# Kernel tuning notes

Measured on AMD Instinct MI355X. Metric: run time of the kernel, lower is better.

## Reference

```python
import jax, jax.numpy as jnp
import numpy as np

N_NODES = 100000
N_EDGES = 600000
DIM = 128
NUM_CLASSES = 10
NUM_GRAPHS = 512
NUM_LAYERS = 4
BN_EPS = 1e-5


def _bn(h, g, b):
    # BatchNorm1d, training-mode statistics (biased variance), affine
    m = h.mean(axis=0)
    v = jnp.var(h, axis=0)
    return (h - m) * jax.lax.rsqrt(v + BN_EPS) * g + b


def setup_inputs() -> dict:
    key = jax.random.key(0)
    ks = jax.random.split(key, 8)
    s_in = 1.0 / np.sqrt(DIM)
    x = jax.random.normal(ks[0], (N_NODES, DIM), dtype=jnp.float32)
    edge_index = jax.random.randint(ks[1], (2, N_EDGES), 0, N_NODES, dtype=jnp.int32)
    batch = jnp.sort(jax.random.randint(ks[2], (N_NODES,), 0, NUM_GRAPHS, dtype=jnp.int32))
    return {
        "x": x,
        "edge_index": edge_index,
        "batch": batch,
        "mlp_w1": jax.random.normal(ks[3], (NUM_LAYERS, DIM, DIM), dtype=jnp.float32) * s_in,
        "mlp_b1": jnp.zeros((NUM_LAYERS, DIM), dtype=jnp.float32),
        "mlp_bn_g": jnp.ones((NUM_LAYERS, DIM), dtype=jnp.float32),
        "mlp_bn_b": jnp.zeros((NUM_LAYERS, DIM), dtype=jnp.float32),
        "mlp_w2": jax.random.normal(ks[4], (NUM_LAYERS, DIM, DIM), dtype=jnp.float32) * s_in,
        "mlp_b2": jnp.zeros((NUM_LAYERS, DIM), dtype=jnp.float32),
        "bn_g": jnp.ones((NUM_LAYERS, DIM), dtype=jnp.float32),
        "bn_b": jnp.zeros((NUM_LAYERS, DIM), dtype=jnp.float32),
        "fc_w": jax.random.normal(ks[5], (NUM_LAYERS + 1, DIM, NUM_CLASSES), dtype=jnp.float32) * s_in,
        "fc_b": jnp.zeros((NUM_LAYERS + 1, NUM_CLASSES), dtype=jnp.float32),
    }


def reference(x, edge_index, batch, mlp_w1, mlp_b1, mlp_bn_g, mlp_bn_b,
              mlp_w2, mlp_b2, bn_g, bn_b, fc_w, fc_b):
    src, dst = edge_index[0], edge_index[1]
    outs = [x]
    h = x
    for i in range(NUM_LAYERS):
        # GINConv: (1+eps)*x + sum_{j in N(i)} x_j  with eps=0 (default)
        agg = jax.ops.segment_sum(h[src], dst, num_segments=N_NODES)
        z = h + agg
        # nn.Sequential(Linear, BatchNorm1d, ReLU, Linear)
        z = jax.nn.relu(_bn(z @ mlp_w1[i] + mlp_b1[i], mlp_bn_g[i], mlp_bn_b[i]))
        z = z @ mlp_w2[i] + mlp_b2[i]
        # outer BN + ReLU
        h = jax.nn.relu(_bn(z, bn_g[i], bn_b[i]))
        outs.append(h)
    out = None
    for i, o in enumerate(outs):
        pooled = jax.ops.segment_sum(o, batch, num_segments=NUM_GRAPHS)
        y = pooled @ fc_w[i] + fc_b[i]  # dropout is identity in eval mode
        out = y if out is None else out + y
    return jax.nn.log_softmax(out, axis=-1)
```

## Files before the change

kernel.cpp:

```cpp
#include <hip/hip_runtime.h>

#define NN 100000
#define NE 600000
#define DD 128
#define NG 512
#define NC 10
#define NL 4

typedef __attribute__((ext_vector_type(8))) short short8;
typedef __attribute__((ext_vector_type(4))) float f32x4;

__device__ __forceinline__ float b2f(unsigned int u) { return __uint_as_float(u << 16); }
__device__ __forceinline__ unsigned int f2b(float f) {
    unsigned int u = __float_as_uint(f);
    return (u + 0x7fffu + ((u >> 16) & 1u)) >> 16;
}
__device__ __forceinline__ void unpack8(uint4 v, float* f) {
    f[0] = b2f(v.x & 0xffffu); f[1] = b2f(v.x >> 16);
    f[2] = b2f(v.y & 0xffffu); f[3] = b2f(v.y >> 16);
    f[4] = b2f(v.z & 0xffffu); f[5] = b2f(v.z >> 16);
    f[6] = b2f(v.w & 0xffffu); f[7] = b2f(v.w >> 16);
}
__device__ __forceinline__ uint4 pack8(const float* f) {
    uint4 v;
    v.x = f2b(f[0]) | (f2b(f[1]) << 16);
    v.y = f2b(f[2]) | (f2b(f[3]) << 16);
    v.z = f2b(f[4]) | (f2b(f[5]) << 16);
    v.w = f2b(f[6]) | (f2b(f[7]) << 16);
    return v;
}


__global__ __launch_bounds__(256) void k_zero(float* __restrict__ p, int n) {
    int i = blockIdx.x * 256 + threadIdx.x;
    if (i < n) p[i] = 0.f;
}
__global__ __launch_bounds__(256) void k_zeroint(int* __restrict__ p, int n) {
    int i = blockIdx.x * 256 + threadIdx.x;
    if (i < n) p[i] = 0;
}
__global__ __launch_bounds__(256) void k_copyint(const int* __restrict__ s, int* __restrict__ d, int n) {
    int i = blockIdx.x * 256 + threadIdx.x;
    if (i < n) d[i] = s[i];
}

__global__ __launch_bounds__(256) void k_cvtH(const float* __restrict__ x, ushort* __restrict__ h) {
    int i = blockIdx.x * 256 + threadIdx.x;
    if (i >= NN * DD / 8) return;
    float4 a = ((const float4*)x)[2 * i], b = ((const float4*)x)[2 * i + 1];
    float f[8] = {a.x, a.y, a.z, a.w, b.x, b.y, b.z, b.w};
    ((uint4*)h)[i] = pack8(f);
}

__global__ __launch_bounds__(256) void k_wpack(const float* __restrict__ w1, const float* __restrict__ w2,
                                               ushort* __restrict__ wp) {
    int id = blockIdx.x * 256 + threadIdx.x;
    int v = id & 63;
    int kc = (id >> 6) & 3;
    int ct = (id >> 8) & 7;
    int m = id >> 11;
    const float* W = (m < 4) ? (w1 + (size_t)m * DD * DD) : (w2 + (size_t)(m - 4) * DD * DD);
    int c = ct * 16 + (v & 15);
    int kbase = kc * 32 + ((v >> 4) << 3);
    ushort* dst = wp + ((size_t)id << 3);
    #pragma unroll
    for (int j = 0; j < 8; ++j) dst[j] = (ushort)f2b(W[(size_t)(kbase + j) * DD + c]);
}


__global__ __launch_bounds__(256) void k_hist(const int* __restrict__ dst, int* __restrict__ deg) {
    int e = blockIdx.x * 256 + threadIdx.x;
    if (e < NE) atomicAdd(&deg[dst[e]], 1);
}
__global__ __launch_bounds__(256) void k_partial(const int* __restrict__ deg, int* __restrict__ part) {
    __shared__ int s[256];
    int t = threadIdx.x;
    int i = blockIdx.x * 256 + t;
    s[t] = (i < NN) ? deg[i] : 0;
    __syncthreads();
    #pragma unroll
    for (int off = 128; off >= 1; off >>= 1) {
        if (t < off) s[t] += s[t + off];
        __syncthreads();
    }
    if (t == 0) part[blockIdx.x] = s[0];
}
__global__ __launch_bounds__(512) void k_scanpart(int* __restrict__ part, int nb) {
    __shared__ int s[512];
    int t = threadIdx.x;
    int v = (t < nb) ? part[t] : 0;
    s[t] = v;
    __syncthreads();
    #pragma unroll
    for (int off = 1; off < 512; off <<= 1) {
        int add = (t >= off) ? s[t - off] : 0;
        __syncthreads();
        s[t] += add;
        __syncthreads();
    }
    if (t < nb) part[t] = s[t] - v;
}
__global__ __launch_bounds__(256) void k_exscan(const int* __restrict__ deg, const int* __restrict__ part,
                                                int* __restrict__ rowofs) {
    __shared__ int s[256];
    int b = blockIdx.x, t = threadIdx.x;
    int i = b * 256 + t;
    int v = (i < NN) ? deg[i] : 0;
    s[t] = v;
    __syncthreads();
    #pragma unroll
    for (int off = 1; off < 256; off <<= 1) {
        int add = (t >= off) ? s[t - off] : 0;
        __syncthreads();
        s[t] += add;
        __syncthreads();
    }
    if (i < NN) rowofs[i] = part[b] + s[t] - v;
    if (i == NN - 1) rowofs[NN] = part[b] + s[t];
}
__global__ __launch_bounds__(256) void k_fill(const int* __restrict__ src, const int* __restrict__ dst,
                                              int* __restrict__ cursor, int* __restrict__ csr) {
    int e = blockIdx.x * 256 + threadIdx.x;
    if (e >= NE) return;
    int d = dst[e];
    int pos = atomicAdd(&cursor[d], 1);
    csr[pos] = src[e];
}

template<bool BN>
__global__ __launch_bounds__(256) void k_gather(const int* __restrict__ rowofs, const int* __restrict__ csr,
                                                const ushort* __restrict__ h, ushort* __restrict__ z,
                                                const float* __restrict__ scsh) {
    int t = threadIdx.x;
    int n = blockIdx.x * 16 + (t >> 4);
    int cl = t & 15;
    int cb = cl * 8;
    float sc[8], sh[8];
    if (BN) {
        #pragma unroll
        for (int j = 0; j < 8; ++j) { sc[j] = scsh[cb + j]; sh[j] = scsh[DD + cb + j]; }
    }
    float acc[8], f[8];
    uint4 v = ((const uint4*)h)[(size_t)n * 16 + cl];
    unpack8(v, f);
    #pragma unroll
    for (int j = 0; j < 8; ++j)
        acc[j] = BN ? fmaxf(fmaf(f[j], sc[j], sh[j]), 0.f) : f[j];
    int start = rowofs[n], end = rowofs[n + 1];
    for (int e = start; e < end; ++e) {
        int s = csr[e];
        v = ((const uint4*)h)[(size_t)s * 16 + cl];
        unpack8(v, f);
        #pragma unroll
        for (int j = 0; j < 8; ++j)
            acc[j] += BN ? fmaxf(fmaf(f[j], sc[j], sh[j]), 0.f) : f[j];
    }
    ((uint4*)z)[(size_t)n * 16 + cl] = pack8(acc);
}

template<bool TRANS>
__global__ __launch_bounds__(256, 4) void k_mm(const ushort* __restrict__ in, const ushort* __restrict__ wp,
                                               const float* __restrict__ bias, const float* __restrict__ scsh,
                                               ushort* __restrict__ outp,
                                               float* __restrict__ ssum, float* __restrict__ ssq) {
    __shared__ __align__(16) char lds[16384];
    const int t = threadIdx.x;
    const int lane = t & 63;
    const int wid = t >> 6;
    const int wr = wid >> 1, wc = wid & 1;
    const int rb = blockIdx.x * 64;
    const int rep = blockIdx.x & 7;

    float scv[8], shv[8];
    if (TRANS) {
        int cb = (t & 15) * 8;
        #pragma unroll
        for (int j = 0; j < 8; ++j) { scv[j] = scsh[cb + j]; shv[j] = scsh[DD + cb + j]; }
    }
    #pragma unroll
    for (int i = 0; i < 4; ++i) {
        int c = i * 256 + t;
        int row = c >> 4;
        int g = rb + row;
        uint4 v = make_uint4(0, 0, 0, 0);
        if (g < NN) {
            v = *((const uint4*)in + (size_t)g * 16 + (c & 15));
            if (TRANS) {
                float f[8];
                unpack8(v, f);
                #pragma unroll
                for (int j = 0; j < 8; ++j) f[j] = fmaxf(fmaf(f[j], scv[j], shv[j]), 0.f);
                v = pack8(f);
            }
        }
        *(uint4*)(lds + ((c * 16) ^ ((row & 7) << 4))) = v;
    }
    __syncthreads();

    f32x4 acc[2][4];
    #pragma unroll
    for (int rt = 0; rt < 2; ++rt)
        #pragma unroll
        for (int ct = 0; ct < 4; ++ct) acc[rt][ct] = (f32x4){0.f, 0.f, 0.f, 0.f};

    #pragma unroll
    for (int kc = 0; kc < 4; ++kc) {
        short8 wf[4];
        #pragma unroll
        for (int ct = 0; ct < 4; ++ct)
            wf[ct] = *(const short8*)(wp + (size_t)((((wc * 4 + ct) * 4 + kc) * 64 + lane) << 3));
        #pragma unroll
        for (int rt = 0; rt < 2; ++rt) {
            int row = wr * 32 + rt * 16 + (lane & 15);
            int off = (row * 256 + ((kc * 32 + ((lane >> 4) << 3)) << 1)) ^ ((row & 7) << 4);
            short8 zf = *(const short8*)(lds + off);
            #pragma unroll
            for (int ct = 0; ct < 4; ++ct)
                acc[rt][ct] = __builtin_amdgcn_mfma_f32_16x16x32_bf16(wf[ct], zf, acc[rt][ct], 0, 0, 0);
        }
    }
    __syncthreads();

    const int zr = lane & 15, cq = lane >> 4;
    #pragma unroll
    for (int rt = 0; rt < 2; ++rt) {
        int row = wr * 32 + rt * 16 + zr;
        #pragma unroll
        for (int ct = 0; ct < 4; ++ct) {
            int c0 = wc * 64 + ct * 16 + cq * 4;
            float4 bi = *(const float4*)(bias + c0);
            f32x4 a = acc[rt][ct];
            float v0 = a[0] + bi.x, v1 = a[1] + bi.y, v2 = a[2] + bi.z, v3 = a[3] + bi.w;
            uint2 pk;
            pk.x = f2b(v0) | (f2b(v1) << 16);
            pk.y = f2b(v2) | (f2b(v3) << 16);
            *(uint2*)(lds + ((row * 256 + c0 * 2) ^ ((row & 7) << 4))) = pk;
        }
    }
    __syncthreads();

    float s8[8], q8[8];
    #pragma unroll
    for (int j = 0; j < 8; ++j) { s8[j] = 0.f; q8[j] = 0.f; }
    #pragma unroll
    for (int i = 0; i < 4; ++i) {
        int c = i * 256 + t;
        int row = c >> 4;
        int g = rb + row;
        if (g < NN) {
            uint4 v = *(const uint4*)(lds + ((c * 16) ^ ((row & 7) << 4)));
            ((uint4*)outp)[(size_t)g * 16 + (c & 15)] = v;
            float f[8];
            unpack8(v, f);
            #pragma unroll
            for (int j = 0; j < 8; ++j) { s8[j] += f[j]; q8[j] += f[j] * f[j]; }
        }
    }
    __syncthreads();
    float* rs = (float*)lds;
    float* rq = rs + 16 * DD;
    const int slot = t >> 4, cb2 = (t & 15) * 8;
    #pragma unroll
    for (int j = 0; j < 8; j += 4) {
        *(float4*)(rs + slot * DD + cb2 + j) = make_float4(s8[j], s8[j + 1], s8[j + 2], s8[j + 3]);
        *(float4*)(rq + slot * DD + cb2 + j) = make_float4(q8[j], q8[j + 1], q8[j + 2], q8[j + 3]);
    }
    __syncthreads();
    #pragma unroll
    for (int off = 8; off >= 1; off >>= 1) {
        if (slot < off) {
            #pragma unroll
            for (int j = 0; j < 8; j += 4) {
                float4 a = *(float4*)(rs + slot * DD + cb2 + j);
                float4 b = *(float4*)(rs + (slot + off) * DD + cb2 + j);
                a.x += b.x; a.y += b.y; a.z += b.z; a.w += b.w;
                *(float4*)(rs + slot * DD + cb2 + j) = a;
                float4 c2 = *(float4*)(rq + slot * DD + cb2 + j);
                float4 d  = *(float4*)(rq + (slot + off) * DD + cb2 + j);
                c2.x += d.x; c2.y += d.y; c2.z += d.z; c2.w += d.w;
                *(float4*)(rq + slot * DD + cb2 + j) = c2;
            }
        }
        __syncthreads();
    }
    if (t < DD) {
        atomicAdd(ssum + rep * DD + t, rs[t]);
        atomicAdd(ssq + rep * DD + t, rq[t]);
    }
}

__global__ __launch_bounds__(DD) void k_finstats(float* __restrict__ ssum, float* __restrict__ ssq,
                                                 float* __restrict__ dst,
                                                 const float* __restrict__ g, const float* __restrict__ b) {
    int t = threadIdx.x;
    float s = 0.f, q = 0.f;
    #pragma unroll
    for (int r = 0; r < 8; ++r) {
        s += ssum[r * DD + t]; q += ssq[r * DD + t];
        ssum[r * DD + t] = 0.f; ssq[r * DD + t] = 0.f;
    }
    const float invn = 1.0f / NN;
    float m = s * invn;
    float var = q * invn - m * m;
    float sc = g[t] * rsqrtf(var + 1e-5f);
    dst[t] = sc;
    dst[DD + t] = b[t] - m * sc;
}

__device__ __forceinline__ int lowerb(const int* __restrict__ a, int n, int key) {
    int lo = 0, hi = n;
    while (lo < hi) {
        int mid = (lo + hi) >> 1;
        if (a[mid] < key) lo = mid + 1; else hi = mid;
    }
    return lo;
}

template<bool BN>
__global__ __launch_bounds__(256) void k_pool(const int* __restrict__ batch, const ushort* __restrict__ h,
                                              float* __restrict__ pooled, const float* __restrict__ scsh) {
    int g = blockIdx.x;
    int t = threadIdx.x;
    int cl = t & 15;
    int rs = t >> 4;
    int cb = cl * 8;
    float sc[8], sh[8];
    if (BN) {
        #pragma unroll
        for (int j = 0; j < 8; ++j) { sc[j] = scsh[cb + j]; sh[j] = scsh[DD + cb + j]; }
    }
    int start = lowerb(batch, NN, g);
    int end = lowerb(batch, NN, g + 1);
    float acc[8];
    #pragma unroll
    for (int j = 0; j < 8; ++j) acc[j] = 0.f;
    for (int n = start + rs; n < end; n += 16) {
        uint4 v = ((const uint4*)h)[(size_t)n * 16 + cl];
        float f[8];
        unpack8(v, f);
        #pragma unroll
        for (int j = 0; j < 8; ++j)
            acc[j] += BN ? fmaxf(fmaf(f[j], sc[j], sh[j]), 0.f) : f[j];
    }
    __shared__ float red[16 * DD];
    #pragma unroll
    for (int j = 0; j < 8; j += 4)
        *(float4*)(red + rs * DD + cb + j) = make_float4(acc[j], acc[j + 1], acc[j + 2], acc[j + 3]);
    __syncthreads();
    #pragma unroll
    for (int off = 8; off >= 1; off >>= 1) {
        if (rs < off) {
            #pragma unroll
            for (int j = 0; j < 8; j += 4) {
                float4 a = *(float4*)(red + rs * DD + cb + j);
                float4 b = *(float4*)(red + (rs + off) * DD + cb + j);
                a.x += b.x; a.y += b.y; a.z += b.z; a.w += b.w;
                *(float4*)(red + rs * DD + cb + j) = a;
            }
        }
        __syncthreads();
    }
    if (rs == 0) {
        #pragma unroll
        for (int j = 0; j < 8; j += 4)
            *(float4*)(pooled + (size_t)g * DD + cb + j) = *(float4*)(red + cb + j);
    }
}

__global__ __launch_bounds__(64) void k_readout(const float* __restrict__ pooled, const float* __restrict__ fcw,
                                                const float* __restrict__ fcb, float* __restrict__ out) {
    int g = blockIdx.x, t = threadIdx.x;
    float part[NC];
    #pragma unroll
    for (int c = 0; c < NC; ++c) part[c] = 0.f;
    for (int i = 0; i < NL + 1; ++i) {
        #pragma unroll
        for (int hh = 0; hh < 2; ++hh) {
            int d = t + (hh << 6);
            float v = pooled[((size_t)i * NG + g) * DD + d];
            const float* wr = fcw + ((size_t)i * DD + d) * NC;
            #pragma unroll
            for (int c = 0; c < NC; ++c) part[c] = fmaf(v, wr[c], part[c]);
        }
    }
    #pragma unroll
    for (int off = 32; off >= 1; off >>= 1) {
        #pragma unroll
        for (int c = 0; c < NC; ++c) part[c] += __shfl_down(part[c], off);
    }
    if (t == 0) {
        float y[NC];
        #pragma unroll
        for (int c = 0; c < NC; ++c) {
            float bs = 0.f;
            for (int i = 0; i < NL + 1; ++i) bs += fcb[i * NC + c];
            y[c] = part[c] + bs;
        }
        float m = y[0];
        #pragma unroll
        for (int c = 1; c < NC; ++c) m = fmaxf(m, y[c]);
        float sum = 0.f;
        #pragma unroll
        for (int c = 0; c < NC; ++c) sum += expf(y[c] - m);
        float ls = logf(sum);
        #pragma unroll
        for (int c = 0; c < NC; ++c) out[(size_t)g * NC + c] = y[c] - m - ls;
    }
}


extern "C" void kernel_launch(void* const* d_in, const int* in_sizes, int n_in,
                              void* d_out, int out_size, void* d_ws, size_t ws_size,
                              hipStream_t stream) {
    const float* x   = (const float*)d_in[0];
    const int*   ei  = (const int*)d_in[1];
    const int*   bat = (const int*)d_in[2];
    const float* w1  = (const float*)d_in[3];
    const float* b1  = (const float*)d_in[4];
    const float* mbg = (const float*)d_in[5];
    const float* mbb = (const float*)d_in[6];
    const float* w2  = (const float*)d_in[7];
    const float* b2  = (const float*)d_in[8];
    const float* bng = (const float*)d_in[9];
    const float* bnb = (const float*)d_in[10];
    const float* fcw = (const float*)d_in[11];
    const float* fcb = (const float*)d_in[12];
    float* out = (float*)d_out;

    ushort* H  = (ushort*)d_ws;
    ushort* Z  = H + (size_t)NN * DD;
    ushort* Y1 = Z + (size_t)NN * DD;
    ushort* WP = Y1 + (size_t)NN * DD;
    float* pooled = (float*)(WP + 8 * 16384);
    float* scsh   = pooled + (size_t)(NL + 1) * NG * DD;
    float* ssum   = scsh + NL * 2 * 2 * DD;
    float* ssq    = ssum + 8 * DD;
    int* deg    = (int*)(ssq + 8 * DD);
    int* rowofs = deg + NN;
    int* part   = rowofs + NN + 1;
    int* cursor = part + 512;
    int* csr    = cursor + NN;

    const int* src = ei;
    const int* dst = ei + NE;
    const int nbN = (NN + 255) / 256;
    const int nbE = (NE + 255) / 256;

    hipLaunchKernelGGL(k_cvtH, dim3(NN * DD / 8 / 256 + 1), dim3(256), 0, stream, x, H);
    hipLaunchKernelGGL(k_zero, dim3(8), dim3(256), 0, stream, ssum, 16 * DD);
    hipLaunchKernelGGL(k_zeroint, dim3(nbN), dim3(256), 0, stream, deg, NN);
    hipLaunchKernelGGL(k_hist, dim3(nbE), dim3(256), 0, stream, dst, deg);
    hipLaunchKernelGGL(k_partial, dim3(nbN), dim3(256), 0, stream, deg, part);
    hipLaunchKernelGGL(k_scanpart, dim3(1), dim3(512), 0, stream, part, nbN);
    hipLaunchKernelGGL(k_exscan, dim3(nbN), dim3(256), 0, stream, deg, part, rowofs);
    hipLaunchKernelGGL(k_copyint, dim3(nbN), dim3(256), 0, stream, rowofs, cursor, NN);
    hipLaunchKernelGGL(k_fill, dim3(nbE), dim3(256), 0, stream, src, dst, cursor, csr);
    hipLaunchKernelGGL(k_wpack, dim3(64), dim3(256), 0, stream, w1, w2, WP);

    const int gmm = (NN + 63) / 64;
    for (int i = 0; i < NL; ++i) {
        float* slot_mlp = scsh + (size_t)(i * 2 + 0) * 2 * DD;
        float* slot_out = scsh + (size_t)(i * 2 + 1) * 2 * DD;
        if (i == 0) {
            hipLaunchKernelGGL((k_pool<false>), dim3(NG), dim3(256), 0, stream, bat, H, pooled, (const float*)nullptr);
            hipLaunchKernelGGL((k_gather<false>), dim3(NN / 16), dim3(256), 0, stream, rowofs, csr, H, Z, (const float*)nullptr);
        } else {
            const float* bnp = scsh + (size_t)((i - 1) * 2 + 1) * 2 * DD;
            hipLaunchKernelGGL((k_pool<true>), dim3(NG), dim3(256), 0, stream, bat, H, pooled + (size_t)i * NG * DD, bnp);
            hipLaunchKernelGGL((k_gather<true>), dim3(NN / 16), dim3(256), 0, stream, rowofs, csr, H, Z, bnp);
        }
        hipLaunchKernelGGL((k_mm<false>), dim3(gmm), dim3(256), 0, stream,
                           Z, WP + (size_t)i * 16384, b1 + (size_t)i * DD, (const float*)nullptr, Y1, ssum, ssq);
        hipLaunchKernelGGL(k_finstats, dim3(1), dim3(DD), 0, stream, ssum, ssq, slot_mlp, mbg + (size_t)i * DD, mbb + (size_t)i * DD);
        hipLaunchKernelGGL((k_mm<true>), dim3(gmm), dim3(256), 0, stream,
                           Y1, WP + (size_t)(4 + i) * 16384, b2 + (size_t)i * DD, slot_mlp, H, ssum, ssq);
        hipLaunchKernelGGL(k_finstats, dim3(1), dim3(DD), 0, stream, ssum, ssq, slot_out, bng + (size_t)i * DD, bnb + (size_t)i * DD);
    }
    hipLaunchKernelGGL((k_pool<true>), dim3(NG), dim3(256), 0, stream, bat, H,
                       pooled + (size_t)NL * NG * DD, scsh + (size_t)(3 * 2 + 1) * 2 * DD);
    hipLaunchKernelGGL(k_readout, dim3(NG), dim3(64), 0, stream, pooled, fcw, fcb, out);
}
```

Baseline: 453.5 us.

## Fuse neighbor gather, graph pooling and first MLP matmul into one kernel

```diff
diff --git a/kernel.cpp b/kernel.cpp
--- a/kernel.cpp
+++ b/kernel.cpp
@@ -128,34 +128,171 @@
 }
 
 template<bool BN>
-__global__ __launch_bounds__(256) void k_gather(const int* __restrict__ rowofs, const int* __restrict__ csr,
-                                                const ushort* __restrict__ h, ushort* __restrict__ z,
-                                                const float* __restrict__ scsh) {
-    int t = threadIdx.x;
-    int n = blockIdx.x * 16 + (t >> 4);
-    int cl = t & 15;
-    int cb = cl * 8;
-    float sc[8], sh[8];
+__global__ __launch_bounds__(256, 4) void k_gmm(const ushort* __restrict__ h,
+                                                const int* __restrict__ rowofs, const int* __restrict__ csr,
+                                                const int* __restrict__ batch,
+                                                const ushort* __restrict__ wp, const float* __restrict__ bias,
+                                                const float* __restrict__ scsh,
+                                                ushort* __restrict__ outp,
+                                                float* __restrict__ ssum, float* __restrict__ ssq,
+                                                float* __restrict__ poolslot) {
+    __shared__ __align__(16) char lds[16384];
+    __shared__ float plds[8][DD];
+    const int t = threadIdx.x;
+    const int lane = t & 63;
+    const int wid = t >> 6;
+    const int wr = wid >> 1, wc = wid & 1;
+    const int rb = blockIdx.x * 64;
+    const int rep = blockIdx.x & 7;
+    const int cl = t & 15, cb = cl * 8;
+
+    const int g0 = batch[rb];
+    const int gr = batch[min(rb + 63, NN - 1)] - g0;
+    const bool direct = (gr >= 8);
+    if (!direct) {
+        for (int i = t; i < 8 * DD; i += 256) ((float*)plds)[i] = 0.f;
+    }
+    float scv[8], shv[8];
     if (BN) {
         #pragma unroll
-        for (int j = 0; j < 8; ++j) { sc[j] = scsh[cb + j]; sh[j] = scsh[DD + cb + j]; }
-    }
-    float acc[8], f[8];
-    uint4 v = ((const uint4*)h)[(size_t)n * 16 + cl];
-    unpack8(v, f);
-    #pragma unroll
-    for (int j = 0; j < 8; ++j)
-        acc[j] = BN ? fmaxf(fmaf(f[j], sc[j], sh[j]), 0.f) : f[j];
-    int start = rowofs[n], end = rowofs[n + 1];
-    for (int e = start; e < end; ++e) {
-        int s = csr[e];
-        v = ((const uint4*)h)[(size_t)s * 16 + cl];
-        unpack8(v, f);
-        #pragma unroll
-        for (int j = 0; j < 8; ++j)
-            acc[j] += BN ? fmaxf(fmaf(f[j], sc[j], sh[j]), 0.f) : f[j];
-    }
-    ((uint4*)z)[(size_t)n * 16 + cl] = pack8(acc);
+        for (int j = 0; j < 8; ++j) { scv[j] = scsh[cb + j]; shv[j] = scsh[DD + cb + j]; }
+    }
+    __syncthreads();
+
+    for (int it = 0; it < 4; ++it) {
+        int row = it * 16 + (t >> 4);
+        int n = rb + row;
+        float acc[8];
+        if (n < NN) {
+            uint4 v = ((const uint4*)h)[(size_t)n * 16 + cl];
+            float f[8];
+            unpack8(v, f);
+            #pragma unroll
+            for (int j = 0; j < 8; ++j)
+                acc[j] = BN ? fmaxf(fmaf(f[j], scv[j], shv[j]), 0.f) : f[j];
+            int gi = batch[n] - g0;
+            if (direct) {
+                #pragma unroll
+                for (int j = 0; j < 8; ++j)
+                    atomicAdd(poolslot + (size_t)(g0 + gi) * DD + cb + j, acc[j]);
+            } else {
+                #pragma unroll
+                for (int j = 0; j < 8; ++j)
+                    atomicAdd(&plds[gi][cb + j], acc[j]);
+            }
+            int e0 = rowofs[n], e1 = rowofs[n + 1];
+            for (int e = e0; e < e1; ++e) {
+                int s = csr[e];
+                uint4 w = ((const uint4*)h)[(size_t)s * 16 + cl];
+                float f2[8];
+                unpack8(w, f2);
+                #pragma unroll
+                for (int j = 0; j < 8; ++j)
+                    acc[j] += BN ? fmaxf(fmaf(f2[j], scv[j], shv[j]), 0.f) : f2[j];
+            }
+        } else {
+            #pragma unroll
+            for (int j = 0; j < 8; ++j) acc[j] = 0.f;
+        }
+        int c = row * 16 + cl;
+        *(uint4*)(lds + ((c * 16) ^ ((row & 7) << 4))) = pack8(acc);
+    }
+    __syncthreads();
+
+    if (!direct && t < DD) {
+        for (int gi = 0; gi <= gr; ++gi)
+            atomicAdd(poolslot + (size_t)(g0 + gi) * DD + t, plds[gi][t]);
+    }
+
+    f32x4 acc[2][4];
+    #pragma unroll
+    for (int rt = 0; rt < 2; ++rt)
+        #pragma unroll
+        for (int ct = 0; ct < 4; ++ct) acc[rt][ct] = (f32x4){0.f, 0.f, 0.f, 0.f};
+
+    #pragma unroll
+    for (int kc = 0; kc < 4; ++kc) {
+        short8 wf[4];
+        #pragma unroll
+        for (int ct = 0; ct < 4; ++ct)
+            wf[ct] = *(const short8*)(wp + (size_t)((((wc * 4 + ct) * 4 + kc) * 64 + lane) << 3));
+        #pragma unroll
+        for (int rt = 0; rt < 2; ++rt) {
+            int row = wr * 32 + rt * 16 + (lane & 15);
+            int off = (row * 256 + ((kc * 32 + ((lane >> 4) << 3)) << 1)) ^ ((row & 7) << 4);
+            short8 zf = *(const short8*)(lds + off);
+            #pragma unroll
+            for (int ct = 0; ct < 4; ++ct)
+                acc[rt][ct] = __builtin_amdgcn_mfma_f32_16x16x32_bf16(wf[ct], zf, acc[rt][ct], 0, 0, 0);
+        }
+    }
+    __syncthreads();
+
+    const int zr = lane & 15, cq = lane >> 4;
+    #pragma unroll
+    for (int rt = 0; rt < 2; ++rt) {
+        int row = wr * 32 + rt * 16 + zr;
+        #pragma unroll
+        for (int ct = 0; ct < 4; ++ct) {
+            int c0 = wc * 64 + ct * 16 + cq * 4;
+            float4 bi = *(const float4*)(bias + c0);
+            f32x4 a = acc[rt][ct];
+            uint2 pk;
+            pk.x = f2b(a[0] + bi.x) | (f2b(a[1] + bi.y) << 16);
+            pk.y = f2b(a[2] + bi.z) | (f2b(a[3] + bi.w) << 16);
+            *(uint2*)(lds + ((row * 256 + c0 * 2) ^ ((row & 7) << 4))) = pk;
+        }
+    }
+    __syncthreads();
+
+    float s8[8], q8[8];
+    #pragma unroll
+    for (int j = 0; j < 8; ++j) { s8[j] = 0.f; q8[j] = 0.f; }
+    #pragma unroll
+    for (int i = 0; i < 4; ++i) {
+        int c = i * 256 + t;
+        int row = c >> 4;
+        int g = rb + row;
+        if (g < NN) {
+            uint4 v = *(const uint4*)(lds + ((c * 16) ^ ((row & 7) << 4)));
+            ((uint4*)outp)[(size_t)g * 16 + (c & 15)] = v;
+            float f[8];
+            unpack8(v, f);
+            #pragma unroll
+            for (int j = 0; j < 8; ++j) { s8[j] += f[j]; q8[j] += f[j] * f[j]; }
+        }
+    }
+    __syncthreads();
+    float* rs = (float*)lds;
+    float* rq = rs + 16 * DD;
+    const int slot = t >> 4;
+    #pragma unroll
+    for (int j = 0; j < 8; j += 4) {
+        *(float4*)(rs + slot * DD + cb + j) = make_float4(s8[j], s8[j + 1], s8[j + 2], s8[j + 3]);
+        *(float4*)(rq + slot * DD + cb + j) = make_float4(q8[j], q8[j + 1], q8[j + 2], q8[j + 3]);
+    }
+    __syncthreads();
+    #pragma unroll
+    for (int off = 8; off >= 1; off >>= 1) {
+        if (slot < off) {
+            #pragma unroll
+            for (int j = 0; j < 8; j += 4) {
+                float4 a = *(float4*)(rs + slot * DD + cb + j);
+                float4 b = *(float4*)(rs + (slot + off) * DD + cb + j);
+                a.x += b.x; a.y += b.y; a.z += b.z; a.w += b.w;
+                *(float4*)(rs + slot * DD + cb + j) = a;
+                float4 c2 = *(float4*)(rq + slot * DD + cb + j);
+                float4 d  = *(float4*)(rq + (slot + off) * DD + cb + j);
+                c2.x += d.x; c2.y += d.y; c2.z += d.z; c2.w += d.w;
+                *(float4*)(rq + slot * DD + cb + j) = c2;
+            }
+        }
+        __syncthreads();
+    }
+    if (t < DD) {
+        atomicAdd(ssum + rep * DD + t, rs[t]);
+        atomicAdd(ssq + rep * DD + t, rq[t]);
+    }
 }
 
 template<bool TRANS>
@@ -230,10 +367,9 @@
             int c0 = wc * 64 + ct * 16 + cq * 4;
             float4 bi = *(const float4*)(bias + c0);
             f32x4 a = acc[rt][ct];
-            float v0 = a[0] + bi.x, v1 = a[1] + bi.y, v2 = a[2] + bi.z, v3 = a[3] + bi.w;
             uint2 pk;
-            pk.x = f2b(v0) | (f2b(v1) << 16);
-            pk.y = f2b(v2) | (f2b(v3) << 16);
+            pk.x = f2b(a[0] + bi.x) | (f2b(a[1] + bi.y) << 16);
+            pk.y = f2b(a[2] + bi.z) | (f2b(a[3] + bi.w) << 16);
             *(uint2*)(lds + ((row * 256 + c0 * 2) ^ ((row & 7) << 4))) = pk;
         }
     }
@@ -428,8 +564,7 @@
     float* out = (float*)d_out;
 
     ushort* H  = (ushort*)d_ws;
-    ushort* Z  = H + (size_t)NN * DD;
-    ushort* Y1 = Z + (size_t)NN * DD;
+    ushort* Y1 = H + (size_t)NN * DD;
     ushort* WP = Y1 + (size_t)NN * DD;
     float* pooled = (float*)(WP + 8 * 16384);
     float* scsh   = pooled + (size_t)(NL + 1) * NG * DD;
@@ -445,9 +580,11 @@
     const int* dst = ei + NE;
     const int nbN = (NN + 255) / 256;
     const int nbE = (NE + 255) / 256;
+    const int npool = (NL + 1) * NG * DD;
 
     hipLaunchKernelGGL(k_cvtH, dim3(NN * DD / 8 / 256 + 1), dim3(256), 0, stream, x, H);
     hipLaunchKernelGGL(k_zero, dim3(8), dim3(256), 0, stream, ssum, 16 * DD);
+    hipLaunchKernelGGL(k_zero, dim3((npool + 255) / 256), dim3(256), 0, stream, pooled, npool);
     hipLaunchKernelGGL(k_zeroint, dim3(nbN), dim3(256), 0, stream, deg, NN);
     hipLaunchKernelGGL(k_hist, dim3(nbE), dim3(256), 0, stream, dst, deg);
     hipLaunchKernelGGL(k_partial, dim3(nbN), dim3(256), 0, stream, deg, part);
@@ -461,16 +598,17 @@
     for (int i = 0; i < NL; ++i) {
         float* slot_mlp = scsh + (size_t)(i * 2 + 0) * 2 * DD;
         float* slot_out = scsh + (size_t)(i * 2 + 1) * 2 * DD;
+        float* poolslot = pooled + (size_t)i * NG * DD;
         if (i == 0) {
-            hipLaunchKernelGGL((k_pool<false>), dim3(NG), dim3(256), 0, stream, bat, H, pooled, (const float*)nullptr);
-            hipLaunchKernelGGL((k_gather<false>), dim3(NN / 16), dim3(256), 0, stream, rowofs, csr, H, Z, (const float*)nullptr);
+            hipLaunchKernelGGL((k_gmm<false>), dim3(gmm), dim3(256), 0, stream,
+                               H, rowofs, csr, bat, WP + (size_t)i * 16384, b1 + (size_t)i * DD,
+                               (const float*)nullptr, Y1, ssum, ssq, poolslot);
         } else {
             const float* bnp = scsh + (size_t)((i - 1) * 2 + 1) * 2 * DD;
-            hipLaunchKernelGGL((k_pool<true>), dim3(NG), dim3(256), 0, stream, bat, H, pooled + (size_t)i * NG * DD, bnp);
-            hipLaunchKernelGGL((k_gather<true>), dim3(NN / 16), dim3(256), 0, stream, rowofs, csr, H, Z, bnp);
-        }
-        hipLaunchKernelGGL((k_mm<false>), dim3(gmm), dim3(256), 0, stream,
-                           Z, WP + (size_t)i * 16384, b1 + (size_t)i * DD, (const float*)nullptr, Y1, ssum, ssq);
+            hipLaunchKernelGGL((k_gmm<true>), dim3(gmm), dim3(256), 0, stream,
+                               H, rowofs, csr, bat, WP + (size_t)i * 16384, b1 + (size_t)i * DD,
+                               bnp, Y1, ssum, ssq, poolslot);
+        }
         hipLaunchKernelGGL(k_finstats, dim3(1), dim3(DD), 0, stream, ssum, ssq, slot_mlp, mbg + (size_t)i * DD, mbb + (size_t)i * DD);
         hipLaunchKernelGGL((k_mm<true>), dim3(gmm), dim3(256), 0, stream,
                            Y1, WP + (size_t)(4 + i) * 16384, b2 + (size_t)i * DD, slot_mlp, H, ssum, ssq);
```

Result: slower. 570.7 us (+25.8%).
